# Optimization experiments

Measured on AMD Instinct MI355X. Metric: run time of the kernel, lower is better.

Reference implementation:

```python
import jax, jax.numpy as jnp
import numpy as np

N = 2048          # total tokens (batch*seq)
H = 4096          # teacher hidden; student hidden = H//2
V = 32000         # vocab
W_HARD = 0.5
W_SOFT = 0.5
BETA = 0.5
IGNORE_INDEX = -100
TEMPERATURE = 2.0


def setup_inputs() -> dict:
    key = jax.random.key(0)
    ks = jax.random.split(key, 7)
    scale_s = 1.0 / np.sqrt(H // 2)
    scale_t = 1.0 / np.sqrt(H)
    return {
        "student_input": jax.random.normal(ks[0], (N, H // 2), jnp.float32),
        "student_weight": jax.random.normal(ks[1], (V, H // 2), jnp.float32) * scale_s,
        "student_bias": jax.random.normal(ks[2], (V,), jnp.float32) * 0.01,
        "teacher_input": jax.random.normal(ks[3], (N, H), jnp.float32),
        "teacher_weight": jax.random.normal(ks[4], (V, H), jnp.float32) * scale_t,
        "teacher_bias": jax.random.normal(ks[5], (V,), jnp.float32) * 0.01,
        "target": jax.random.randint(ks[6], (N,), 0, V, jnp.int64),
    }


def _jsd_lm_head_loss(student_input, student_weight, student_bias,
                      teacher_input, teacher_weight, teacher_bias, target):
    # linear heads: [N, V]
    s_logits = student_input @ student_weight.T + student_bias
    t_logits = teacher_input @ teacher_weight.T + teacher_bias

    n_total = target.shape[0]

    # hard loss: CE on un-tempered student logits, sum over valid, / total tokens
    s_logp_ce = jax.nn.log_softmax(s_logits.astype(jnp.float32), axis=-1)
    valid = target != IGNORE_INDEX
    safe_tgt = jnp.where(valid, target, 0)
    nll = -jnp.take_along_axis(s_logp_ce, safe_tgt[:, None], axis=1)[:, 0]
    hard_loss = jnp.sum(jnp.where(valid, nll, 0.0)) / n_total

    # soft loss: generalized JSD on temperature-scaled logits
    sp = jax.nn.log_softmax((s_logits / TEMPERATURE).astype(jnp.float32), axis=-1)
    tp = jax.nn.log_softmax((t_logits / TEMPERATURE).astype(jnp.float32), axis=-1)
    # mixture m = beta * p_student + (1-beta) * p_teacher (symmetric at beta=0.5)
    log_m = jnp.log(BETA * jnp.exp(sp) + (1.0 - BETA) * jnp.exp(tp))
    kl_s = jnp.sum(jnp.exp(sp) * (sp - log_m))   # KL(student || m), sum-reduced
    kl_t = jnp.sum(jnp.exp(tp) * (tp - log_m))   # KL(teacher || m), sum-reduced
    jsd = BETA * kl_s + (1.0 - BETA) * kl_t
    soft_loss = jsd / n_total

    return W_HARD * hard_loss + W_SOFT * soft_loss


def reference(student_input, student_weight, student_bias,
              teacher_input, teacher_weight, teacher_bias, target):
    return _jsd_lm_head_loss(student_input, student_weight, student_bias,
                             teacher_input, teacher_weight, teacher_bias, target)
```

## Files before the change

kernel.cpp:

```cpp
#include <hip/hip_runtime.h>
#include <hip/hip_bf16.h>
#include <cstdint>
#include <cstddef>

typedef __attribute__((ext_vector_type(8))) short short8v;
typedef __attribute__((ext_vector_type(4))) int   i32x4;

__device__ __forceinline__ short f2bf(float f) {
    union { float f; unsigned u; } c; c.f = f;
    unsigned r = c.u + 0x7FFFu + ((c.u >> 16) & 1u);
    return (short)(r >> 16);
}

__device__ __forceinline__ float bf2f(ushort u) {
    union { unsigned u; float f; } c; c.u = ((unsigned)u) << 16;
    return c.f;
}

__device__ __forceinline__ void load_lds_16B(const void* g, void* l) {
    __builtin_amdgcn_global_load_lds(
        (const __attribute__((address_space(1))) void*)g,
        (__attribute__((address_space(3))) void*)l, 16, 0, 0);
}

__global__ __launch_bounds__(256)
void quant_all_kernel(const float* __restrict__ s_in, const float* __restrict__ t_in,
                      const float* __restrict__ s_w,  const float* __restrict__ t_w,
                      uint8_t* __restrict__ s_in_q, uint8_t* __restrict__ t_in_q,
                      uint8_t* __restrict__ s_w_q,  uint8_t* __restrict__ t_w_q,
                      float* __restrict__ sa_s, float* __restrict__ sa_t,
                      float* __restrict__ sw_s, float* __restrict__ sw_t,
                      double* __restrict__ accum)
{
    const int b = blockIdx.x;
    if (b == 0 && threadIdx.x == 0) { accum[0] = 0.0; accum[1] = 0.0; }

    const float* src; uint8_t* dst; float* sc; int R, row;
    if (b < 2048)       { src = s_in; dst = s_in_q; sc = sa_s; R = 2048; row = b; }
    else if (b < 4096)  { src = t_in; dst = t_in_q; sc = sa_t; R = 4096; row = b - 2048; }
    else if (b < 36096) { src = s_w;  dst = s_w_q;  sc = sw_s; R = 2048; row = b - 4096; }
    else                { src = t_w;  dst = t_w_q;  sc = sw_t; R = 4096; row = b - 36096; }

    const int tid = threadIdx.x;
    const float* x = src + (size_t)row * R;
    const int ng = R >> 10;

    float4 v[4];
    float am = 0.f;
#pragma unroll
    for (int g = 0; g < 4; ++g) {
        if (g < ng) {
            v[g] = *reinterpret_cast<const float4*>(&x[g * 1024 + tid * 4]);
            am = fmaxf(am, fmaxf(fmaxf(fabsf(v[g].x), fabsf(v[g].y)),
                                 fmaxf(fabsf(v[g].z), fabsf(v[g].w))));
        }
    }
#pragma unroll
    for (int off = 32; off > 0; off >>= 1)
        am = fmaxf(am, __shfl_xor(am, off));
    __shared__ float wam[4];
    if ((tid & 63) == 0) wam[tid >> 6] = am;
    __syncthreads();
    am = fmaxf(fmaxf(wam[0], wam[1]), fmaxf(wam[2], wam[3]));
    am = fmaxf(am, 1e-20f);
    const float inv = 127.0f / am;
    if (tid == 0) sc[row] = am / 127.0f;

    uint32_t* out = (uint32_t*)(dst + (size_t)row * R);
#pragma unroll
    for (int g = 0; g < 4; ++g) {
        if (g < ng) {
            int q0 = __float2int_rn(v[g].x * inv);
            int q1 = __float2int_rn(v[g].y * inv);
            int q2 = __float2int_rn(v[g].z * inv);
            int q3 = __float2int_rn(v[g].w * inv);
            q0 = min(127, max(-127, q0)); q1 = min(127, max(-127, q1));
            q2 = min(127, max(-127, q2)); q3 = min(127, max(-127, q3));
            out[g * 256 + tid] = (q0 & 255) | ((q1 & 255) << 8) |
                                 ((q2 & 255) << 16) | ((uint32_t)(q3 & 255) << 24);
        }
    }
}


#define SEG_A0 0
#define SEG_A1 32768
#define SEG_B0 65536
#define SEG_B1 98304

#define READ_B_ALL(bseg) do {                                                  \
    _Pragma("unroll")                                                          \
    for (int nf = 0; nf < 4; ++nf) {                                           \
        const int rb = (bseg) + brow + nf * 2048;                              \
        bfr[nf][0] = *(const i32x4*)&sh[rb + c16a];                            \
        bfr[nf][1] = *(const i32x4*)&sh[rb + c16b];                            \
    }                                                                          \
} while (0)

#define READ_A2(aseg, mfb) do {                                                \
    _Pragma("unroll")                                                          \
    for (int d = 0; d < 2; ++d) {                                              \
        const int ra = (aseg) + arow + ((mfb) + d) * 2048;                     \
        af[d][0] = *(const i32x4*)&sh[ra + c16a];                              \
        af[d][1] = *(const i32x4*)&sh[ra + c16b];                              \
    }                                                                          \
} while (0)

#define MFMA16(mfb) do {                                                       \
    __builtin_amdgcn_s_setprio(1);                                             \
    _Pragma("unroll")                                                          \
    for (int d = 0; d < 2; ++d) {                                              \
        _Pragma("unroll")                                                      \
        for (int nf = 0; nf < 4; ++nf) {                                       \
            acc[(mfb)+d][nf] = __builtin_amdgcn_mfma_i32_16x16x64_i8(          \
                af[d][0], bfr[nf][0], acc[(mfb)+d][nf], 0, 0, 0);              \
            acc[(mfb)+d][nf] = __builtin_amdgcn_mfma_i32_16x16x64_i8(          \
                af[d][1], bfr[nf][1], acc[(mfb)+d][nf], 0, 0, 0);              \
        }                                                                      \
    }                                                                          \
    __builtin_amdgcn_s_setprio(0);                                             \
} while (0)

#define BAR() __builtin_amdgcn_s_barrier()
#define VMCNT4() asm volatile("s_waitcnt vmcnt(4)" ::: "memory")
#define VMCNT0() asm volatile("s_waitcnt vmcnt(0)" ::: "memory")

__global__ __launch_bounds__(512, 2)
void gemm256_i8_kernel(const uint8_t* __restrict__ A, const uint8_t* __restrict__ W,
                       const float* __restrict__ sa, const float* __restrict__ sw,
                       const float* __restrict__ bias, ushort* __restrict__ C,
                       int K, int V)
{
    __shared__ uint8_t sh[131072];
    ushort* shs = (ushort*)sh;

    const int tid  = threadIdx.x;
    const int lane = tid & 63;
    const int wave = tid >> 6;
    const int wm = wave >> 2;
    const int wn = wave & 3;

    const int cpx = gridDim.x >> 3;
    const int wg  = ((int)blockIdx.x & 7) * cpx + ((int)blockIdx.x >> 3);
    const int row0 = (wg & 7) * 256;
    const int col0 = (wg >> 3) * 256;

    const int NT = K >> 7;
    const int NI = NT >> 1;

    const int sr  = lane >> 3;
    const int scb = ((lane & 7) ^ sr) * 16;
    const size_t a_off = (size_t)(row0 + wave * 8 + sr) * K + scb;
    const size_t w_off = (size_t)(col0 + wave * 8 + sr) * K + scb;
    const int lds_u = wave * 1024;

    auto stage_half = [&](const uint8_t* gb, size_t goff, int seg, int h, int k0) {
        const uint8_t* g0 = gb + goff + (size_t)(h * 128) * K + k0;
        load_lds_16B(g0,                  &sh[seg + h * 16384 + lds_u]);
        load_lds_16B(g0 + (size_t)64 * K, &sh[seg + h * 16384 + 8192 + lds_u]);
    };

    const int l15  = lane & 15;
    const int c16a = (((lane >> 4)    ) ^ (lane & 7)) * 16;
    const int c16b = (((lane >> 4) + 4) ^ (lane & 7)) * 16;
    const int arow = (wm * 128 + l15) * 128;
    const int brow = (wn * 64  + l15) * 128;

    i32x4 acc[8][4];
#pragma unroll
    for (int m = 0; m < 8; ++m)
#pragma unroll
        for (int n = 0; n < 4; ++n)
            acc[m][n] = (i32x4)(0);

    i32x4 bfr[4][2];
    i32x4 af[2][2];

    stage_half(A, a_off, SEG_A0, 0, 0);
    stage_half(A, a_off, SEG_A0, 1, 0);
    stage_half(W, w_off, SEG_B0, 0, 0);
    stage_half(W, w_off, SEG_B0, 1, 0);
    stage_half(W, w_off, SEG_B1, 0, 128);
    stage_half(W, w_off, SEG_B1, 1, 128);
    VMCNT4();
    BAR();

    for (int i = 0; i < NI - 1; ++i) {
        const int kA1 = (2 * i + 1) * 128;
        const int kN2 = (2 * i + 2) * 128;
        const int kB3 = (2 * i + 3) * 128;

        READ_B_ALL(SEG_B0); READ_A2(SEG_A0, 0);
        stage_half(A, a_off, SEG_A1, 0, kA1);
        BAR(); MFMA16(0); BAR();

        READ_A2(SEG_A0, 2);
        stage_half(A, a_off, SEG_A1, 1, kA1);
        BAR(); MFMA16(2); BAR();

        READ_A2(SEG_A0, 4);
        stage_half(W, w_off, SEG_B0, 0, kN2);
        BAR(); MFMA16(4); BAR();

        READ_A2(SEG_A0, 6);
        stage_half(W, w_off, SEG_B0, 1, kN2);
        BAR(); MFMA16(6);
        VMCNT4();
        BAR();

        READ_B_ALL(SEG_B1); READ_A2(SEG_A1, 0);
        stage_half(A, a_off, SEG_A0, 0, kN2);
        BAR(); MFMA16(0); BAR();

        READ_A2(SEG_A1, 2);
        stage_half(A, a_off, SEG_A0, 1, kN2);
        BAR(); MFMA16(2); BAR();

        READ_A2(SEG_A1, 4);
        stage_half(W, w_off, SEG_B1, 0, kB3);
        BAR(); MFMA16(4); BAR();

        READ_A2(SEG_A1, 6);
        stage_half(W, w_off, SEG_B1, 1, kB3);
        BAR(); MFMA16(6);
        VMCNT4();
        BAR();
    }

    {
        const int kA1 = (NT - 1) * 128;
        READ_B_ALL(SEG_B0); READ_A2(SEG_A0, 0);
        stage_half(A, a_off, SEG_A1, 0, kA1);
        BAR(); MFMA16(0); BAR();
        READ_A2(SEG_A0, 2);
        stage_half(A, a_off, SEG_A1, 1, kA1);
        BAR(); MFMA16(2); BAR();
        READ_A2(SEG_A0, 4); BAR(); MFMA16(4); BAR();
        READ_A2(SEG_A0, 6); BAR(); MFMA16(6);
        VMCNT0();
        BAR();
        READ_B_ALL(SEG_B1); READ_A2(SEG_A1, 0); BAR(); MFMA16(0); BAR();
        READ_A2(SEG_A1, 2); BAR(); MFMA16(2); BAR();
        READ_A2(SEG_A1, 4); BAR(); MFMA16(4); BAR();
        READ_A2(SEG_A1, 6); BAR(); MFMA16(6);
    }

    float bb[4], swv[4];
#pragma unroll
    for (int nf = 0; nf < 4; ++nf) {
        const int gc = col0 + wn * 64 + nf * 16 + l15;
        bb[nf]  = bias[gc];
        swv[nf] = sw[gc];
    }

    __syncthreads();
#pragma unroll
    for (int mf = 0; mf < 8; ++mf) {
        const int rl = wm * 128 + mf * 16 + (lane >> 4) * 4;
        const float4 sav = *reinterpret_cast<const float4*>(&sa[row0 + rl]);
        const float* savp = (const float*)&sav;
#pragma unroll
        for (int nf = 0; nf < 4; ++nf) {
            const int cl = wn * 64 + nf * 16 + l15;
#pragma unroll
            for (int j = 0; j < 4; ++j) {
                const int row = rl + j;
                const float v = (float)acc[mf][nf][j] * (savp[j] * swv[nf]) + bb[nf];
                const int pc = (((cl >> 3) ^ (((row >> 2) & 3) << 1)) << 3) + (cl & 7);
                shs[row * 256 + pc] = (ushort)f2bf(v);
            }
        }
    }
    __syncthreads();
#pragma unroll
    for (int pass = 0; pass < 16; ++pass) {
        const int r = pass * 16 + (tid >> 5);
        const int pc16 = (tid & 31) ^ (((r >> 2) & 3) << 1);
        *reinterpret_cast<short8v*>(&C[(size_t)(row0 + r) * V + col0 + (tid & 31) * 8]) =
            *reinterpret_cast<const short8v*>(&shs[r * 256 + pc16 * 8]);
    }
}

__global__ __launch_bounds__(1024)
void stats_loss_kernel(const ushort* __restrict__ S, const ushort* __restrict__ Tm,
                       const int* __restrict__ tgt, double* __restrict__ accum, int V)
{
    const int r = blockIdx.x;
    const ushort* s = S  + (size_t)r * V;
    const ushort* t = Tm + (size_t)r * V;
    const int tid = threadIdx.x;

    short8v sv[4], tv[4];
    bool valid[4];

    float ms = -1e30f, l1 = 0.f, lh = 0.f;
    float mt = -1e30f, lt = 0.f;
#pragma unroll
    for (int it = 0; it < 4; ++it) {
        const int v = it * 8192 + tid * 8;
        valid[it] = (v < V);
        if (valid[it]) {
            sv[it] = *reinterpret_cast<const short8v*>(&s[v]);
            tv[it] = *reinterpret_cast<const short8v*>(&t[v]);
#pragma unroll
            for (int j = 0; j < 8; ++j) {
                float x = bf2f((ushort)sv[it][j]);
                if (x > ms) {
                    float eh = __expf(0.5f * (ms - x));
                    lh *= eh; l1 *= eh * eh; ms = x;
                }
                float e = __expf(0.5f * (x - ms));
                lh += e; l1 += e * e;
                float y = bf2f((ushort)tv[it][j]);
                if (y > mt) {
                    lt *= __expf(0.5f * (mt - y));
                    mt = y;
                }
                lt += __expf(0.5f * (y - mt));
            }
        }
    }
#pragma unroll
    for (int off = 32; off > 0; off >>= 1) {
        float mso = __shfl_xor(ms, off), l1o = __shfl_xor(l1, off), lho = __shfl_xor(lh, off);
        float mn = fmaxf(ms, mso);
        float ea = __expf(0.5f * (ms - mn)), eb = __expf(0.5f * (mso - mn));
        lh = lh * ea + lho * eb;
        l1 = l1 * ea * ea + l1o * eb * eb;
        ms = mn;
        float mto = __shfl_xor(mt, off), lto = __shfl_xor(lt, off);
        float mn2 = fmaxf(mt, mto);
        lt = lt * __expf(0.5f * (mt - mn2)) + lto * __expf(0.5f * (mto - mn2));
        mt = mn2;
    }
    __shared__ float red[16][5];
    __shared__ float bc[3];
    if ((tid & 63) == 0) {
        int w = tid >> 6;
        red[w][0] = ms; red[w][1] = l1; red[w][2] = lh;
        red[w][3] = mt; red[w][4] = lt;
    }
    __syncthreads();
    if (tid == 0) {
        float M = red[0][0], L1 = red[0][1], LH = red[0][2];
        float Mt = red[0][3], Lt = red[0][4];
#pragma unroll
        for (int w = 1; w < 16; ++w) {
            float mn = fmaxf(M, red[w][0]);
            float ea = __expf(0.5f * (M - mn)), eb = __expf(0.5f * (red[w][0] - mn));
            LH = LH * ea + red[w][2] * eb;
            L1 = L1 * ea * ea + red[w][1] * eb * eb;
            M = mn;
            float mn2 = fmaxf(Mt, red[w][3]);
            Lt = Lt * __expf(0.5f * (Mt - mn2)) + red[w][4] * __expf(0.5f * (red[w][3] - mn2));
            Mt = mn2;
        }
        bc[0] = M + __logf(L1);
        bc[1] = 0.5f * M + __logf(LH);
        bc[2] = 0.5f * Mt + __logf(Lt);
    }
    __syncthreads();
    const float ls1 = bc[0], ls2 = bc[1], lt2 = bc[2];

    float local = 0.f;
#pragma unroll
    for (int it = 0; it < 4; ++it) {
        if (valid[it]) {
#pragma unroll
            for (int j = 0; j < 8; ++j) {
                float sp = 0.5f * bf2f((ushort)sv[it][j]) - ls2;
                float tp = 0.5f * bf2f((ushort)tv[it][j]) - lt2;
                float p = __expf(sp), q = __expf(tp);
                float mm = 0.5f * (p + q);
                float lm = __logf(fmaxf(mm, 1e-38f));
                local += 0.5f * (p * (sp - lm) + q * (tp - lm));
            }
        }
    }
#pragma unroll
    for (int off = 32; off > 0; off >>= 1)
        local += __shfl_xor(local, off);
    __shared__ float ls[16];
    if ((tid & 63) == 0) ls[tid >> 6] = local;
    __syncthreads();
    if (tid == 0) {
        float blocksum = 0.f;
#pragma unroll
        for (int w = 0; w < 16; ++w) blocksum += ls[w];
        atomicAdd(&accum[1], (double)blocksum);
        int tg = tgt[r];
        if (tg != -100) {
            float nll = -(bf2f(s[tg]) - ls1);
            atomicAdd(&accum[0], (double)nll);
        }
    }
}

__global__ void finalize_kernel(const double* __restrict__ accum,
                                float* __restrict__ out, double inv_n) {
    out[0] = (float)(0.5 * (accum[0] * inv_n) + 0.5 * (accum[1] * inv_n));
}

extern "C" void kernel_launch(void* const* d_in, const int* in_sizes, int n_in,
                              void* d_out, int out_size, void* d_ws, size_t ws_size,
                              hipStream_t stream)
{
    const float* s_in = (const float*)d_in[0];
    const float* s_w  = (const float*)d_in[1];
    const float* s_b  = (const float*)d_in[2];
    const float* t_in = (const float*)d_in[3];
    const float* t_w  = (const float*)d_in[4];
    const float* t_b  = (const float*)d_in[5];
    const int*   tgt  = (const int*)d_in[6];

    const int N = 2048, V = 32000, KS = 2048, KT = 4096;

    const size_t e_sin = (size_t)N * KS;
    const size_t e_sw  = (size_t)V * KS;
    const size_t e_tin = (size_t)N * KT;
    const size_t e_tw  = (size_t)V * KT;

    char* ws = (char*)d_ws;
    double* accum = (double*)ws;

    float* sa_s = (float*)(ws + 4096);
    float* sa_t = sa_s + 2048;
    float* sw_s = sa_t + 2048;
    float* sw_t = sw_s + 32000;
    uint8_t* s_in_q = (uint8_t*)(ws + 278528);
    uint8_t* s_w_q  = s_in_q + e_sin;
    uint8_t* t_in_q = s_w_q + e_sw;
    uint8_t* t_w_q  = t_in_q + e_tin;
    ushort* s_log = (ushort*)(t_w_q + e_tw);
    ushort* t_log = s_log + (size_t)N * V;

    quant_all_kernel<<<68096, 256, 0, stream>>>(
        s_in, t_in, s_w, t_w,
        s_in_q, t_in_q, s_w_q, t_w_q,
        sa_s, sa_t, sw_s, sw_t, accum);

    const int grid = (V / 256) * (N / 256);
    gemm256_i8_kernel<<<grid, 512, 0, stream>>>(t_in_q, t_w_q, sa_t, sw_t, t_b, t_log, KT, V);
    gemm256_i8_kernel<<<grid, 512, 0, stream>>>(s_in_q, s_w_q, sa_s, sw_s, s_b, s_log, KS, V);

    stats_loss_kernel<<<N, 1024, 0, stream>>>(s_log, t_log, tgt, accum, V);

    finalize_kernel<<<1, 1, 0, stream>>>(accum, (float*)d_out, 1.0 / (double)N);
}
```

Before: 712.3 us.

## Fuse softmax row-sum statistics into GEMM epilogue and merge both GEMM launches

The GEMM epilogue now computes exp(v/2) and exp(v) per logit, reduces them across lanes and atomically adds them into per-row sum buffers. This removes the online max/sum pass from the loss kernel, which now only does the JSD pass using precomputed log-sums. The teacher and student GEMMs are also merged into one launch, split by block index, and the quant kernel zeroes the sum buffers. The sums skip max subtraction, so they could overflow for large logits, and float atomics make the result order-dependent.

```diff
diff --git a/kernel.cpp b/kernel.cpp
--- a/kernel.cpp
+++ b/kernel.cpp
@@ -30,10 +30,16 @@
                       uint8_t* __restrict__ s_w_q,  uint8_t* __restrict__ t_w_q,
                       float* __restrict__ sa_s, float* __restrict__ sa_t,
                       float* __restrict__ sw_s, float* __restrict__ sw_t,
-                      double* __restrict__ accum)
+                      float* __restrict__ sums, double* __restrict__ accum)
 {
     const int b = blockIdx.x;
-    if (b == 0 && threadIdx.x == 0) { accum[0] = 0.0; accum[1] = 0.0; }
+    const int tid = threadIdx.x;
+    if (b == 0) {
+        if (tid == 0) { accum[0] = 0.0; accum[1] = 0.0; }
+#pragma unroll
+        for (int k = 0; k < 24; ++k)
+            sums[tid * 24 + k] = 0.0f;
+    }
 
     const float* src; uint8_t* dst; float* sc; int R, row;
     if (b < 2048)       { src = s_in; dst = s_in_q; sc = sa_s; R = 2048; row = b; }
@@ -41,7 +47,6 @@
     else if (b < 36096) { src = s_w;  dst = s_w_q;  sc = sw_s; R = 2048; row = b - 4096; }
     else                { src = t_w;  dst = t_w_q;  sc = sw_t; R = 4096; row = b - 36096; }
 
-    const int tid = threadIdx.x;
     const float* x = src + (size_t)row * R;
     const int ng = R >> 10;
 
@@ -126,10 +131,15 @@
 #define VMCNT0() asm volatile("s_waitcnt vmcnt(0)" ::: "memory")
 
 __global__ __launch_bounds__(512, 2)
-void gemm256_i8_kernel(const uint8_t* __restrict__ A, const uint8_t* __restrict__ W,
-                       const float* __restrict__ sa, const float* __restrict__ sw,
-                       const float* __restrict__ bias, ushort* __restrict__ C,
-                       int K, int V)
+void gemm256_i8_seq_kernel(const uint8_t* __restrict__ At, const uint8_t* __restrict__ Wt,
+                           const float* __restrict__ sat, const float* __restrict__ swt,
+                           const float* __restrict__ bt,  ushort* __restrict__ Ct,
+                           float* __restrict__ sumh_t,
+                           const uint8_t* __restrict__ As, const uint8_t* __restrict__ Ws,
+                           const float* __restrict__ sas, const float* __restrict__ sws,
+                           const float* __restrict__ bs,  ushort* __restrict__ Cs,
+                           float* __restrict__ sumh_s, float* __restrict__ sum1_s,
+                           int V)
 {
     __shared__ uint8_t sh[131072];
     ushort* shs = (ushort*)sh;
@@ -140,10 +150,20 @@
     const int wm = wave >> 2;
     const int wn = wave & 3;
 
-    const int cpx = gridDim.x >> 3;
-    const int wg  = ((int)blockIdx.x & 7) * cpx + ((int)blockIdx.x >> 3);
+    const int half = (int)(gridDim.x >> 1);
+    const int cpx  = half >> 3;
+    const bool teacher = (int)blockIdx.x < half;
+    const int b2 = teacher ? (int)blockIdx.x : (int)blockIdx.x - half;
+    const int wg = (b2 & 7) * cpx + (b2 >> 3);
     const int row0 = (wg & 7) * 256;
     const int col0 = (wg >> 3) * 256;
+
+    const uint8_t* A; const uint8_t* W; const float* sa; const float* sw;
+    const float* bias; ushort* C; float* sumh; float* sum1; int K;
+    if (teacher) { A = At; W = Wt; sa = sat; sw = swt; bias = bt; C = Ct;
+                   sumh = sumh_t; sum1 = nullptr; K = 4096; }
+    else         { A = As; W = Ws; sa = sas; sw = sws; bias = bs; C = Cs;
+                   sumh = sumh_s; sum1 = sum1_s; K = 2048; }
 
     const int NT = K >> 7;
     const int NI = NT >> 1;
@@ -260,14 +280,27 @@
         const float4 sav = *reinterpret_cast<const float4*>(&sa[row0 + rl]);
         const float* savp = (const float*)&sav;
 #pragma unroll
-        for (int nf = 0; nf < 4; ++nf) {
-            const int cl = wn * 64 + nf * 16 + l15;
-#pragma unroll
-            for (int j = 0; j < 4; ++j) {
-                const int row = rl + j;
+        for (int j = 0; j < 4; ++j) {
+            const int row = rl + j;
+            float ph = 0.f, p1 = 0.f;
+#pragma unroll
+            for (int nf = 0; nf < 4; ++nf) {
+                const int cl = wn * 64 + nf * 16 + l15;
                 const float v = (float)acc[mf][nf][j] * (savp[j] * swv[nf]) + bb[nf];
+                const float e = __expf(0.5f * v);
+                ph += e;
+                p1 += e * e;
                 const int pc = (((cl >> 3) ^ (((row >> 2) & 3) << 1)) << 3) + (cl & 7);
                 shs[row * 256 + pc] = (ushort)f2bf(v);
+            }
+#pragma unroll
+            for (int m = 1; m < 16; m <<= 1) {
+                ph += __shfl_xor(ph, m);
+                p1 += __shfl_xor(p1, m);
+            }
+            if (l15 == 0) {
+                atomicAdd(&sumh[row0 + row], ph);
+                if (sum1) atomicAdd(&sum1[row0 + row], p1);
             }
         }
     }
@@ -282,94 +315,31 @@
 }
 
 __global__ __launch_bounds__(1024)
-void stats_loss_kernel(const ushort* __restrict__ S, const ushort* __restrict__ Tm,
-                       const int* __restrict__ tgt, double* __restrict__ accum, int V)
+void jsd_kernel(const ushort* __restrict__ S, const ushort* __restrict__ Tm,
+                const float* __restrict__ sum1_s, const float* __restrict__ sumh_s,
+                const float* __restrict__ sumh_t, const int* __restrict__ tgt,
+                double* __restrict__ accum, int V)
 {
     const int r = blockIdx.x;
     const ushort* s = S  + (size_t)r * V;
     const ushort* t = Tm + (size_t)r * V;
     const int tid = threadIdx.x;
 
-    short8v sv[4], tv[4];
-    bool valid[4];
-
-    float ms = -1e30f, l1 = 0.f, lh = 0.f;
-    float mt = -1e30f, lt = 0.f;
+    const float ls1 = __logf(sum1_s[r]);
+    const float ls2 = __logf(sumh_s[r]);
+    const float lt2 = __logf(sumh_t[r]);
+
+    float local = 0.f;
 #pragma unroll
     for (int it = 0; it < 4; ++it) {
         const int v = it * 8192 + tid * 8;
-        valid[it] = (v < V);
-        if (valid[it]) {
-            sv[it] = *reinterpret_cast<const short8v*>(&s[v]);
-            tv[it] = *reinterpret_cast<const short8v*>(&t[v]);
+        if (v < V) {
+            short8v sv = *reinterpret_cast<const short8v*>(&s[v]);
+            short8v tv = *reinterpret_cast<const short8v*>(&t[v]);
 #pragma unroll
             for (int j = 0; j < 8; ++j) {
-                float x = bf2f((ushort)sv[it][j]);
-                if (x > ms) {
-                    float eh = __expf(0.5f * (ms - x));
-                    lh *= eh; l1 *= eh * eh; ms = x;
-                }
-                float e = __expf(0.5f * (x - ms));
-                lh += e; l1 += e * e;
-                float y = bf2f((ushort)tv[it][j]);
-                if (y > mt) {
-                    lt *= __expf(0.5f * (mt - y));
-                    mt = y;
-                }
-                lt += __expf(0.5f * (y - mt));
-            }
-        }
-    }
-#pragma unroll
-    for (int off = 32; off > 0; off >>= 1) {
-        float mso = __shfl_xor(ms, off), l1o = __shfl_xor(l1, off), lho = __shfl_xor(lh, off);
-        float mn = fmaxf(ms, mso);
-        float ea = __expf(0.5f * (ms - mn)), eb = __expf(0.5f * (mso - mn));
-        lh = lh * ea + lho * eb;
-        l1 = l1 * ea * ea + l1o * eb * eb;
-        ms = mn;
-        float mto = __shfl_xor(mt, off), lto = __shfl_xor(lt, off);
-        float mn2 = fmaxf(mt, mto);
-        lt = lt * __expf(0.5f * (mt - mn2)) + lto * __expf(0.5f * (mto - mn2));
-        mt = mn2;
-    }
-    __shared__ float red[16][5];
-    __shared__ float bc[3];
-    if ((tid & 63) == 0) {
-        int w = tid >> 6;
-        red[w][0] = ms; red[w][1] = l1; red[w][2] = lh;
-        red[w][3] = mt; red[w][4] = lt;
-    }
-    __syncthreads();
-    if (tid == 0) {
-        float M = red[0][0], L1 = red[0][1], LH = red[0][2];
-        float Mt = red[0][3], Lt = red[0][4];
-#pragma unroll
-        for (int w = 1; w < 16; ++w) {
-            float mn = fmaxf(M, red[w][0]);
-            float ea = __expf(0.5f * (M - mn)), eb = __expf(0.5f * (red[w][0] - mn));
-            LH = LH * ea + red[w][2] * eb;
-            L1 = L1 * ea * ea + red[w][1] * eb * eb;
-            M = mn;
-            float mn2 = fmaxf(Mt, red[w][3]);
-            Lt = Lt * __expf(0.5f * (Mt - mn2)) + red[w][4] * __expf(0.5f * (red[w][3] - mn2));
-            Mt = mn2;
-        }
-        bc[0] = M + __logf(L1);
-        bc[1] = 0.5f * M + __logf(LH);
-        bc[2] = 0.5f * Mt + __logf(Lt);
-    }
-    __syncthreads();
-    const float ls1 = bc[0], ls2 = bc[1], lt2 = bc[2];
-
-    float local = 0.f;
-#pragma unroll
-    for (int it = 0; it < 4; ++it) {
-        if (valid[it]) {
-#pragma unroll
-            for (int j = 0; j < 8; ++j) {
-                float sp = 0.5f * bf2f((ushort)sv[it][j]) - ls2;
-                float tp = 0.5f * bf2f((ushort)tv[it][j]) - lt2;
+                float sp = 0.5f * bf2f((ushort)sv[j]) - ls2;
+                float tp = 0.5f * bf2f((ushort)tv[j]) - lt2;
                 float p = __expf(sp), q = __expf(tp);
                 float mm = 0.5f * (p + q);
                 float lm = __logf(fmaxf(mm, 1e-38f));
@@ -427,7 +397,10 @@
     float* sa_t = sa_s + 2048;
     float* sw_s = sa_t + 2048;
     float* sw_t = sw_s + 32000;
-    uint8_t* s_in_q = (uint8_t*)(ws + 278528);
+    float* sum1_s = (float*)(ws + 276480);
+    float* sumh_s = sum1_s + 2048;
+    float* sumh_t = sumh_s + 2048;
+    uint8_t* s_in_q = (uint8_t*)(ws + 303104);
     uint8_t* s_w_q  = s_in_q + e_sin;
     uint8_t* t_in_q = s_w_q + e_sw;
     uint8_t* t_w_q  = t_in_q + e_tin;
@@ -437,13 +410,14 @@
     quant_all_kernel<<<68096, 256, 0, stream>>>(
         s_in, t_in, s_w, t_w,
         s_in_q, t_in_q, s_w_q, t_w_q,
-        sa_s, sa_t, sw_s, sw_t, accum);
-
-    const int grid = (V / 256) * (N / 256);
-    gemm256_i8_kernel<<<grid, 512, 0, stream>>>(t_in_q, t_w_q, sa_t, sw_t, t_b, t_log, KT, V);
-    gemm256_i8_kernel<<<grid, 512, 0, stream>>>(s_in_q, s_w_q, sa_s, sw_s, s_b, s_log, KS, V);
-
-    stats_loss_kernel<<<N, 1024, 0, stream>>>(s_log, t_log, tgt, accum, V);
+        sa_s, sa_t, sw_s, sw_t, sum1_s, accum);
+
+    const int grid = 2 * (V / 256) * (N / 256);
+    gemm256_i8_seq_kernel<<<grid, 512, 0, stream>>>(
+        t_in_q, t_w_q, sa_t, sw_t, t_b, t_log, sumh_t,
+        s_in_q, s_w_q, sa_s, sw_s, s_b, s_log, sumh_s, sum1_s, V);
+
+    jsd_kernel<<<N, 1024, 0, stream>>>(s_log, t_log, sum1_s, sumh_s, sumh_t, tgt, accum, V);
 
     finalize_kernel<<<1, 1, 0, stream>>>(accum, (float*)d_out, 1.0 / (double)N);
 }
```

Result: faster. 681.7 us, median of 2 (-4.3%).
